# Kernel tuning notes

Hardware: AMD Instinct MI355X
Metric: run time of the kernel (lower is better)

Reference implementation:

```python
import jax, jax.numpy as jnp
import numpy as np

BS, S, N, C, H, CP, T, CT, NB = 1, 2, 2048, 128, 8, 16, 512, 384, 3
DH = C // H
INF = 1.0e8

def _ln(x, w, b, eps=1e-5):
    mu = jnp.mean(x, axis=-1, keepdims=True)
    var = jnp.var(x, axis=-1, keepdims=True)
    return (x - mu) * jax.lax.rsqrt(var + eps) * w + b

def _ln_na(x, eps=1e-5):
    mu = jnp.mean(x, axis=-1, keepdims=True)
    var = jnp.var(x, axis=-1, keepdims=True)
    return (x - mu) * jax.lax.rsqrt(var + eps)

def _betas(n):
    # query row l belongs to window centered at 32*(l//32)+16; keys within +/- n_keys//2=64
    l = jnp.arange(n)
    centers = (l // 32) * 32 + 16
    m = jnp.arange(n)
    ok = (m[None, :] >= (centers - 64)[:, None]) & (m[None, :] < (centers + 64)[:, None])
    return jnp.where(ok, 0.0, -INF).astype(jnp.float32)

def setup_inputs():
    key = jax.random.key(0)
    ks = iter(jax.random.split(key, 80))
    def W(*shape):
        return jax.random.normal(next(ks), shape, dtype=jnp.float32) * 0.05
    return {
        "atom_single": jax.random.normal(next(ks), (BS, S, N, C), dtype=jnp.float32),
        "atom_proj": jax.random.normal(next(ks), (BS, N, C), dtype=jnp.float32),
        "atom_pair": jax.random.normal(next(ks), (BS, N, N, CP), dtype=jnp.float32),
        "mask": jnp.ones((BS, N), jnp.float32),
        "tok_idx": jnp.sort(jax.random.randint(next(ks), (BS, N), 0, T), axis=-1),
        "aln_s_w": jnp.ones((NB, C), jnp.float32), "aln_s_b": jnp.zeros((NB, C), jnp.float32),
        "aln_gate_w": W(NB, C, C), "aln_gate_b": jnp.zeros((NB, C), jnp.float32),
        "aln_shift_w": W(NB, C, C),
        "q_w": W(NB, C, C), "q_b": jnp.zeros((NB, C), jnp.float32),
        "k_w": W(NB, C, C), "v_w": W(NB, C, C),
        "pair_ln_w": jnp.ones((NB, CP), jnp.float32), "pair_ln_b": jnp.zeros((NB, CP), jnp.float32),
        "pair_w": W(NB, CP, H),
        "gate_w": W(NB, C, C), "out_w": W(NB, C, C),
        "og_w": W(NB, C, C), "og_b": jnp.full((NB, C), -2.0, jnp.float32),
        "t_aln_s_w": jnp.ones((NB, C), jnp.float32), "t_aln_s_b": jnp.zeros((NB, C), jnp.float32),
        "t_aln_gate_w": W(NB, C, C), "t_aln_gate_b": jnp.zeros((NB, C), jnp.float32),
        "t_aln_shift_w": W(NB, C, C),
        "t_a_w": W(NB, C, 2 * C), "t_b_w": W(NB, C, 2 * C),
        "t_out_w": W(NB, 2 * C, C),
        "t_og_w": W(NB, C, C), "t_og_b": jnp.full((NB, C), -2.0, jnp.float32),
        "tok_w": W(C, CT),
    }

def _forward(atom_single, atom_proj, atom_pair, mask, tok_idx, aln_s_w, aln_s_b, aln_gate_w, aln_gate_b, aln_shift_w, q_w, q_b, k_w, v_w, pair_ln_w, pair_ln_b, pair_w, gate_w, out_w, og_w, og_b, t_aln_s_w, t_aln_s_b, t_aln_gate_w, t_aln_gate_b, t_aln_shift_w, t_a_w, t_b_w, t_out_w, t_og_w, t_og_b, tok_w):
    betas = _betas(N)[None, None, None]                        # [1,1,1,N,N]
    mask_bias = ((mask - 1.0) * INF)[:, None, None, None, :]   # [bs,1,1,1,N]
    s = atom_proj[:, None]                                     # [bs,1,N,C]
    a = atom_single                                            # [bs,S,N,C]
    for i in range(NB):
        # AttentionPairBias with AdaLN conditioning on s
        sn = _ln(s, aln_s_w[i], aln_s_b[i])
        a1 = jax.nn.sigmoid(sn @ aln_gate_w[i] + aln_gate_b[i]) * _ln_na(a) + sn @ aln_shift_w[i]
        q = (a1 @ q_w[i] + q_b[i]).reshape(BS, S, N, H, DH)
        k = (a1 @ k_w[i]).reshape(BS, S, N, H, DH)
        v = (a1 @ v_w[i]).reshape(BS, S, N, H, DH)
        zb = _ln(atom_pair, pair_ln_w[i], pair_ln_b[i]) @ pair_w[i]    # [bs,N,N,H]
        zb = jnp.transpose(zb, (0, 3, 1, 2))[:, None]                  # [bs,1,H,N,N]
        logits = jnp.einsum('bsqhd,bskhd->bshqk', q, k) / np.float32(np.sqrt(DH)) + zb + betas + mask_bias
        p = jax.nn.softmax(logits, axis=-1)
        o = jnp.einsum('bshqk,bskhd->bsqhd', p, v).reshape(BS, S, N, C)
        o = (jax.nn.sigmoid(a1 @ gate_w[i]) * o) @ out_w[i]
        a = a + jax.nn.sigmoid(sn @ og_w[i] + og_b[i]) * o
        # ConditionedTransitionBlock (SwiGLU with adaLN-Zero gating)
        sn2 = _ln(s, t_aln_s_w[i], t_aln_s_b[i])
        a2 = jax.nn.sigmoid(sn2 @ t_aln_gate_w[i] + t_aln_gate_b[i]) * _ln_na(a) + sn2 @ t_aln_shift_w[i]
        hidden = jax.nn.silu(a2 @ t_a_w[i]) * (a2 @ t_b_w[i])
        a = a + jax.nn.sigmoid(sn2 @ t_og_w[i] + t_og_b[i]) * (hidden @ t_out_w[i])
    # project to token dim, relu, scatter-mean atoms -> tokens
    q_tok = jax.nn.relu(a @ tok_w)                             # [bs,S,N,CT]
    oh = jax.nn.one_hot(tok_idx, T, dtype=q_tok.dtype)         # [bs,N,T]
    cnt = jnp.clip(jnp.sum(oh, axis=1), 1.0)                   # [bs,T]
    tok = jnp.einsum('bsnc,bnt->bstc', q_tok, oh) / cnt[:, None, :, None]
    return tok

def reference(atom_single, atom_proj, atom_pair, mask, tok_idx, aln_s_w, aln_s_b, aln_gate_w, aln_gate_b, aln_shift_w, q_w, q_b, k_w, v_w, pair_ln_w, pair_ln_b, pair_w, gate_w, out_w, og_w, og_b, t_aln_s_w, t_aln_s_b, t_aln_gate_w, t_aln_gate_b, t_aln_shift_w, t_a_w, t_b_w, t_out_w, t_og_w, t_og_b, tok_w):
    return _forward(atom_single, atom_proj, atom_pair, mask, tok_idx, aln_s_w, aln_s_b, aln_gate_w, aln_gate_b, aln_shift_w, q_w, q_b, k_w, v_w, pair_ln_w, pair_ln_b, pair_w, gate_w, out_w, og_w, og_b, t_aln_s_w, t_aln_s_b, t_aln_gate_w, t_aln_gate_b, t_aln_shift_w, t_a_w, t_b_w, t_out_w, t_og_w, t_og_b, tok_w)
```

## Files before the change

### kernel.cpp

```cpp
#include <hip/hip_runtime.h>
#include <math.h>

#define NATOM 2048
#define CD 128
#define SD 2
#define TT 512
#define CTD 384
#define NBI 3
#define MR 4096

typedef unsigned short ushortx;
typedef __attribute__((ext_vector_type(8))) short bf16x8;
typedef __attribute__((ext_vector_type(4))) float f32x4;
typedef __attribute__((ext_vector_type(4))) unsigned short us4;

__device__ __forceinline__ float sigm(float x){ return 1.0f/(1.0f+expf(-x)); }
__device__ __forceinline__ ushortx f2b(float f){
  union { float f; unsigned u; } v; v.f = f;
  unsigned r = v.u + 0x7fffu + ((v.u>>16)&1u);
  return (ushortx)(r>>16);
}
__device__ __forceinline__ float b2f(ushortx u){
  union { unsigned u; float f; } v; v.u = ((unsigned)u)<<16; return v.f;
}
union U8 { ushortx u[8]; float4 v; };

__device__ __forceinline__ void unpack8(float* dst, float4 v){
  U8 pk; pk.v = v;
  #pragma unroll
  for (int t=0;t<8;t++) dst[t] = b2f(pk.u[t]);
}

#define OFFB_W3T    0ll
#define OFFB_B3     589824ll
#define OFFB_WQKVGT 599040ll
#define OFFB_BQ     992256ll
#define OFFB_WOUTT  998400ll
#define OFFB_WABT   1096704ll
#define OFFB_WTOUTT 1489920ll
#define OFFB_WTOKT  1686528ll
#define OFFB_A1     1784832ll
#define OFFB_SNP    2833408ll
#define OFFB_A      12270592ll
#define OFFB_QKVG   14367744ll
#define OFFB_ZB     18562048ll
#define OFFB_QTOK   31144960ll

struct WPtrs {
  const float *aln_gate_w, *aln_gate_b, *aln_shift_w, *og_w, *og_b;
  const float *t_aln_gate_w, *t_aln_gate_b, *t_aln_shift_w, *t_og_w, *t_og_b;
  const float *q_w, *q_b, *k_w, *v_w, *gate_w, *out_w;
  const float *t_a_w, *t_b_w, *t_out_w, *tok_w;
};

__global__ __launch_bounds__(256) void prologue_kernel(WPtrs P, char* __restrict__ wsb,
  const float* __restrict__ atom_single, const float* __restrict__ atom_pair,
  const float* __restrict__ plw, const float* __restrict__ plb, const float* __restrict__ pw)
{
  int b = blockIdx.x;
  if (b < 3471){
    long long idx = (long long)b*256 + threadIdx.x;
    const long long s0=294912, s1=2304, s2=196608, s3=1536, s4=49152, s5=196608, s6=98304;
    if (idx < s0) {
      int which = (int)(idx/49152); int r = (int)(idx%49152); int n=r/128, k=r%128;
      int i = which>>1, t = which&1;
      const float* src;
      if (n<128)      src = (t?P.t_aln_gate_w :P.aln_gate_w ) + i*16384 + k*128 + n;
      else if (n<256) src = (t?P.t_aln_shift_w:P.aln_shift_w) + i*16384 + k*128 + (n-128);
      else            src = (t?P.t_og_w       :P.og_w       ) + i*16384 + k*128 + (n-256);
      ((ushortx*)(wsb+OFFB_W3T))[idx] = f2b(*src); return;
    }
    idx -= s0;
    if (idx < s1) {
      int which = (int)(idx/384); int col = (int)(idx%384); int i=which>>1, t=which&1;
      float v = 0.f;
      if (col<128)       v = (t?P.t_aln_gate_b:P.aln_gate_b)[i*128+col];
      else if (col>=256) v = (t?P.t_og_b      :P.og_b      )[i*128+col-256];
      ((float*)(wsb+OFFB_B3))[idx] = v; return;
    }
    idx -= s1;
    if (idx < s2) {
      int i = (int)(idx/65536); int r = (int)(idx%65536); int n=r/128, k=r%128;
      int seg = n>>7, c = n&127;
      const float* src = (seg==0?P.q_w: seg==1?P.k_w: seg==2?P.v_w: P.gate_w) + i*16384 + k*128 + c;
      ((ushortx*)(wsb+OFFB_WQKVGT))[idx] = f2b(*src); return;
    }
    idx -= s2;
    if (idx < s3) {
      int i = (int)(idx/512); int col = (int)(idx%512);
      ((float*)(wsb+OFFB_BQ))[idx] = (col<128) ? P.q_b[i*128+col] : 0.f; return;
    }
    idx -= s3;
    if (idx < s4) {
      int i = (int)(idx/16384); int r = (int)(idx%16384); int n=r/128, k=r%128;
      ((ushortx*)(wsb+OFFB_WOUTT))[idx] = f2b(P.out_w[i*16384 + k*128 + n]); return;
    }
    idx -= s4;
    if (idx < s5) {
      int i = (int)(idx/65536); int r = (int)(idx%65536); int n=r/128, k=r%128;
      const float* src = (n<256) ? P.t_a_w + i*32768 + k*256 + n
                                 : P.t_b_w + i*32768 + k*256 + (n-256);
      ((ushortx*)(wsb+OFFB_WABT))[idx] = f2b(*src); return;
    }
    idx -= s5;
    if (idx < s6) {
      int i = (int)(idx/32768); int r = (int)(idx%32768); int n=r/256, k=r%256;
      ((ushortx*)(wsb+OFFB_WTOUTT))[idx] = f2b(P.t_out_w[i*32768 + k*128 + n]); return;
    }
    idx -= s6;
    {
      int n = (int)(idx/128); int k = (int)(idx%128);
      ((ushortx*)(wsb+OFFB_WTOKT))[idx] = f2b(P.tok_w[k*384 + n]); return;
    }
  }
  if (b < 5519){
    int i = (b-3471)*256 + threadIdx.x;
    ((float*)(wsb+OFFB_A))[i] = atom_single[i];
    return;
  }
  {
    int idx = (b-5519)*256 + threadIdx.x;
    int q = idx>>7, j = idx&127;
    int m = (q & ~31) - 48 + j;
    bool ok = (m>=0 && m<NATOM);
    float x[16]; float mu=0.f, rs=0.f;
    if (ok){
      float s=0.f, sq=0.f;
      const float* p = atom_pair + ((long long)q*NATOM + m)*16;
      #pragma unroll
      for (int c=0;c<16;c++){ x[c]=p[c]; s+=x[c]; sq+=x[c]*x[c]; }
      mu = s*(1.f/16.f); float var = sq*(1.f/16.f)-mu*mu; rs = rsqrtf(var+1e-5f);
    }
    ushortx* zb = (ushortx*)(wsb+OFFB_ZB);
    #pragma unroll
    for (int it=0; it<NBI; it++){
      float out[8] = {0,0,0,0,0,0,0,0};
      if (ok){
        #pragma unroll
        for (int c=0;c<16;c++){
          float xn = (x[c]-mu)*rs*plw[it*16+c] + plb[it*16+c];
          #pragma unroll
          for (int h=0;h<8;h++) out[h] += xn * pw[it*128 + c*8 + h];
        }
      }
      #pragma unroll
      for (int h=0;h<8;h++)
        zb[(((long long)it*8+h)*NATOM + q)*128 + j] = f2b(out[h]);
    }
  }
}

__global__ __launch_bounds__(256) void attn_kernel(const ushortx* __restrict__ qkvg,
  const ushortx* __restrict__ zb, const float* __restrict__ mask, ushortx* __restrict__ og)
{
  int qb = blockIdx.x, h = blockIdx.y, s = blockIdx.z;
  int base = qb*32 - 48;
  __shared__ __align__(16) float Qs[32][20];
  __shared__ __align__(16) ushortx KsU[128][24];
  __shared__ __align__(16) ushortx VsU[128][24];
  __shared__ __align__(16) float Ls[32][132];
  __shared__ float maskb[128], redx[32][8], rowv[32];
  int tid = threadIdx.x;
  for (int idx=tid; idx<32*2; idx+=256){
    int r=idx>>1, d8=(idx&1)*8;
    float4 v = *(const float4*)&qkvg[((long long)(s*NATOM + qb*32 + r))*512 + h*16 + d8];
    unpack8(&Qs[r][d8], v);
  }
  for (int idx=tid; idx<512; idx+=256){
    int j = idx&127, d8 = ((idx>>7)&1)*8, kv = idx>>8;
    int m = base + j; int mc = m<0?0:(m>NATOM-1?NATOM-1:m);
    long long row = ((long long)(s*NATOM + mc))*512;
    float4 v = *(const float4*)&qkvg[row + (kv?256:128) + h*16 + d8];
    if (kv) *(float4*)&VsU[j][d8] = v; else *(float4*)&KsU[j][d8] = v;
  }
  if (tid < 128){
    int m = base + tid;
    maskb[tid] = (m>=0 && m<NATOM) ? (mask[m]-1.0f)*1e8f : -1e30f;
  }
  __syncthreads();
  int r = tid>>3, g = tid&7;
  {
    float4 q0=*(float4*)&Qs[r][0], q1=*(float4*)&Qs[r][4], q2=*(float4*)&Qs[r][8], q3=*(float4*)&Qs[r][12];
    const ushortx* zrow = zb + ((long long)h*NATOM + (qb*32+r))*128;
    #pragma unroll
    for (int j=g; j<128; j+=8){
      U8 ka, kb; ka.v = *(const float4*)&KsU[j][0]; kb.v = *(const float4*)&KsU[j][8];
      float dot = q0.x*b2f(ka.u[0]) + q0.y*b2f(ka.u[1]) + q0.z*b2f(ka.u[2]) + q0.w*b2f(ka.u[3])
                + q1.x*b2f(ka.u[4]) + q1.y*b2f(ka.u[5]) + q1.z*b2f(ka.u[6]) + q1.w*b2f(ka.u[7])
                + q2.x*b2f(kb.u[0]) + q2.y*b2f(kb.u[1]) + q2.z*b2f(kb.u[2]) + q2.w*b2f(kb.u[3])
                + q3.x*b2f(kb.u[4]) + q3.y*b2f(kb.u[5]) + q3.z*b2f(kb.u[6]) + q3.w*b2f(kb.u[7]);
      Ls[r][j] = dot*0.25f + b2f(zrow[j]) + maskb[j];
    }
  }
  __syncthreads();
  float pmax = -1e30f;
  for (int j=g*16; j<g*16+16; j++) pmax = fmaxf(pmax, Ls[r][j]);
  redx[r][g] = pmax; __syncthreads();
  if (g==0){ float mx=redx[r][0]; for(int u=1;u<8;u++) mx=fmaxf(mx,redx[r][u]); rowv[r]=mx; }
  __syncthreads();
  float mx = rowv[r];
  float psum = 0.f;
  for (int j=g*16; j<g*16+16; j++){ float e = expf(Ls[r][j]-mx); Ls[r][j]=e; psum += e; }
  redx[r][g] = psum; __syncthreads();
  if (g==0){ float sm=0.f; for(int u=0;u<8;u++) sm+=redx[r][u]; rowv[r]=sm; }
  __syncthreads();
  {
    int q2=tid>>3, dg=(tid>>1)&3, jh=tid&1;
    float4 acc = make_float4(0.f,0.f,0.f,0.f);
    for (int j=jh*64; j<jh*64+64; j++){
      float p = Ls[q2][j];
      us4 vv = *(const us4*)&VsU[j][dg*4];
      acc.x += p*b2f(vv[0]); acc.y += p*b2f(vv[1]);
      acc.z += p*b2f(vv[2]); acc.w += p*b2f(vv[3]);
    }
    acc.x += __shfl_xor(acc.x,1); acc.y += __shfl_xor(acc.y,1);
    acc.z += __shfl_xor(acc.z,1); acc.w += __shfl_xor(acc.w,1);
    if (jh==0){
      long long mrow = (long long)(s*NATOM + qb*32 + q2);
      float inv = 1.0f / rowv[q2];
      us4 gt = *(const us4*)&qkvg[mrow*512 + 384 + h*16 + dg*4];
      us4 st;
      st[0] = f2b(sigm(b2f(gt[0]))*acc.x*inv);
      st[1] = f2b(sigm(b2f(gt[1]))*acc.y*inv);
      st[2] = f2b(sigm(b2f(gt[2]))*acc.z*inv);
      st[3] = f2b(sigm(b2f(gt[3]))*acc.w*inv);
      *(us4*)(og + mrow*128 + h*16 + dg*4) = st;
    }
  }
}

template<int LAST>
__global__ __launch_bounds__(256) void postattn_kernel(
  float* __restrict__ Af, const ushortx* __restrict__ A1,
  const ushortx* __restrict__ Wout,
  const ushortx* __restrict__ Wab,
  const ushortx* __restrict__ Wtout,
  const ushortx* __restrict__ WN,
  const float*   __restrict__ biasN,
  const ushortx* __restrict__ snpA,
  const ushortx* __restrict__ snpT,
  const ushortx* __restrict__ snpN,
  ushortx* __restrict__ QKVG,
  float*   __restrict__ QTOK)
{
  __shared__ __align__(16) ushortx Bt[2][64][136];
  __shared__ __align__(16) float   Afr[16][132];
  __shared__ __align__(16) ushortx A2t[16][136];
  __shared__ __align__(16) ushortx Ht[16][264];
  __shared__ __align__(16) ushortx XX[16*264];
  ushortx (*A1t)[136] = (ushortx(*)[136])XX;
  ushortx (*Hs)[264]  = (ushortx(*)[264])XX;

  int tid=threadIdx.x, rowBase=blockIdx.x*16;
  int wave=tid>>6, lane=tid&63, lr=lane&15, lk=(lane>>4)*8;
  int wc = wave*16;
  int r=tid>>4, c8=(tid&15)*8;
  long long grow = rowBase + r;
  int sr=tid>>2, csB=(tid&3)*32;
  int crow = (lane>>4)*4;

  *(float4*)&A1t[r][c8] = *(const float4*)&A1[grow*128 + c8];
  { const float4* ap=(const float4*)&Af[grow*128+c8];
    *(float4*)&Afr[r][c8]=ap[0]; *(float4*)&Afr[r][c8+4]=ap[1]; }
  const int NP = LAST ? 20 : 22;
  {
    const float4* bg = (const float4*)(Wout + (long long)sr*128 + csB);
    #pragma unroll
    for (int u=0;u<4;u++) *(float4*)&Bt[0][sr][csB+u*8] = bg[u];
  }
  f32x4 acc = (f32x4){0.f,0.f,0.f,0.f};
  for (int p=0; p<NP; p++){
    __syncthreads();
    if (p+1 < NP){
      int pn = p+1;
      const ushortx* bsrc; long long bstride;
      if (pn<2)      { bsrc = Wout  + (long long)(pn*64)*128;                      bstride=128; }
      else if (pn<10){ bsrc = Wab   + (long long)((pn-2)*64)*128;                  bstride=128; }
      else if (pn<14){ int q=pn-10; bsrc = Wtout + (long long)((q>>1)*64)*256 + (q&1)*128; bstride=256; }
      else           { int q=pn-14; bsrc = WN    + (long long)(q*64)*128;          bstride=128; }
      const float4* bg=(const float4*)(bsrc + (long long)sr*bstride + csB);
      #pragma unroll
      for (int u=0;u<4;u++) *(float4*)&Bt[pn&1][sr][csB+u*8] = bg[u];
    }
    if (p==2){
      float x[8], s=0.f, sq=0.f;
      #pragma unroll
      for (int u=0;u<8;u++){ x[u]=Afr[r][c8+u]; s+=x[u]; sq+=x[u]*x[u]; }
      #pragma unroll
      for (int off=1; off<16; off<<=1){ s+=__shfl_xor(s,off); sq+=__shfl_xor(sq,off); }
      float mu=s*(1.f/128.f), rs=rsqrtf(sq*(1.f/128.f)-mu*mu+1e-5f);
      const ushortx* sp = snpT + (long long)(grow&2047)*384;
      U8 ga,ha,pk; ga.v=*(const float4*)&sp[c8]; ha.v=*(const float4*)&sp[128+c8];
      #pragma unroll
      for (int t=0;t<8;t++) pk.u[t]=f2b(sigm(b2f(ga.u[t]))*((x[t]-mu)*rs)+b2f(ha.u[t]));
      *(float4*)&A2t[r][c8]=pk.v;
      __syncthreads();
    }
    if (p==14){
      float x[8], s=0.f, sq=0.f;
      #pragma unroll
      for (int u=0;u<8;u++){ x[u]=Afr[r][c8+u]; s+=x[u]; sq+=x[u]*x[u]; }
      { float4* ap=(float4*)&Af[grow*128+c8];
        ap[0]=*(float4*)&Afr[r][c8]; ap[1]=*(float4*)&Afr[r][c8+4]; }
      if (LAST){
        U8 pk;
        #pragma unroll
        for (int t=0;t<8;t++) pk.u[t]=f2b(x[t]);
        *(float4*)&A2t[r][c8]=pk.v;
      } else {
        #pragma unroll
        for (int off=1; off<16; off<<=1){ s+=__shfl_xor(s,off); sq+=__shfl_xor(sq,off); }
        float mu=s*(1.f/128.f), rs=rsqrtf(sq*(1.f/128.f)-mu*mu+1e-5f);
        const ushortx* sp = snpN + (long long)(grow&2047)*384;
        U8 ga,ha,pk; ga.v=*(const float4*)&sp[c8]; ha.v=*(const float4*)&sp[128+c8];
        #pragma unroll
        for (int t=0;t<8;t++) pk.u[t]=f2b(sigm(b2f(ga.u[t]))*((x[t]-mu)*rs)+b2f(ha.u[t]));
        *(float4*)&A2t[r][c8]=pk.v;
      }
      __syncthreads();
    }
    if (p!=11 && p!=13) acc=(f32x4){0.f,0.f,0.f,0.f};
    #pragma unroll
    for (int ks=0; ks<4; ks++){
      bf16x8 a;
      if (p<2)       a = *(const bf16x8*)&A1t[lr][ks*32+lk];
      else if (p<10) a = *(const bf16x8*)&A2t[lr][ks*32+lk];
      else if (p<14){ int kc=(p-10)&1; a = *(const bf16x8*)&Hs[lr][kc*128+ks*32+lk]; }
      else           a = *(const bf16x8*)&A2t[lr][ks*32+lk];
      bf16x8 b = *(const bf16x8*)&Bt[p&1][wc+lr][ks*32+lk];
      acc = __builtin_amdgcn_mfma_f32_16x16x32_bf16(a,b,acc,0,0,0);
    }
    if (p<2){
      int ccol = p*64 + wc + lr;
      #pragma unroll
      for (int rr=0;rr<4;rr++){
        int rrow=crow+rr;
        float g=b2f(snpA[(long long)((rowBase+rrow)&2047)*384 + 256 + ccol]);
        Afr[rrow][ccol]+=sigm(g)*acc[rr];
      }
    } else if (p<10){
      int cp=p-2; int ccol=cp*64+wc+lr;
      if (cp<4){
        #pragma unroll
        for (int rr=0;rr<4;rr++) Ht[crow+rr][ccol]=f2b(acc[rr]);
      } else {
        int hc=ccol-256;
        #pragma unroll
        for (int rr=0;rr<4;rr++){
          float ha=b2f(Ht[crow+rr][hc]);
          Hs[crow+rr][hc]=f2b(ha*sigm(ha)*acc[rr]);
        }
      }
    } else if (p==11 || p==13){
      int cp=(p-10)>>1; int ccol=cp*64+wc+lr;
      #pragma unroll
      for (int rr=0;rr<4;rr++){
        int rrow=crow+rr;
        float g=b2f(snpT[(long long)((rowBase+rrow)&2047)*384 + 256 + ccol]);
        Afr[rrow][ccol]+=sigm(g)*acc[rr];
      }
    } else if (p>=14){
      int q=p-14; int ccol=q*64+wc+lr;
      if (LAST){
        #pragma unroll
        for (int rr=0;rr<4;rr++)
          QTOK[(long long)(rowBase+crow+rr)*384 + ccol]=fmaxf(acc[rr],0.f);
      } else {
        float bv=biasN[ccol];
        #pragma unroll
        for (int rr=0;rr<4;rr++)
          QKVG[(long long)(rowBase+crow+rr)*512 + ccol]=f2b(acc[rr]+bv);
      }
    }
  }
}

template<int AM, int BM>
__global__ __launch_bounds__(256) void gemm_f(
    const void* __restrict__ Asrc, long long strideA,
    const ushortx* __restrict__ B, long long strideB,
    const float* __restrict__ bias, long long strideBias,
    void* Cv, long long strideC,
    int M, int N, int K, int mode,
    const ushortx* __restrict__ gate, int gate_ld, int gate_coloff,
    const void* __restrict__ p1, const void* __restrict__ p2,
    const void* __restrict__ p3, const void* __restrict__ p4)
{
  constexpr int CG  = 256/BM;
  constexpr int XC  = 128/CG;
  constexpr int F4  = XC/8;
  constexpr int ACI = BM/32;
  int z = blockIdx.z;
  B += z*strideB;
  if (bias) bias += z*strideBias;
  float* C = (float*)Cv + z*strideC;
  ushortx* Cu = (ushortx*)Cv + z*strideC;
  __shared__ __align__(16) ushortx At[BM][136];
  __shared__ __align__(16) ushortx Bt[64][136];
  int tid = threadIdx.x;
  int rowBase = blockIdx.y*BM, colBase = blockIdx.x*64;
  int wave = tid>>6, lane = tid&63;
  int wr = (wave>>1)*(BM/2), wc = (wave&1)*32;
  int lr = lane&15, lk = (lane>>4)*8;
  f32x4 acc[ACI][2];
  #pragma unroll
  for (int i=0;i<ACI;i++)
    #pragma unroll
    for (int j=0;j<2;j++) acc[i][j] = (f32x4){0.f,0.f,0.f,0.f};

  int sr = tid/CG, q = tid%CG, cs = q*XC;
  int row = rowBase + sr;
  int bsr = tid>>2, bq = tid&3, bcs = bq*32;

  for (int kc=0; kc<K; kc+=128){
    if (kc) __syncthreads();
    if (AM==0){
      const ushortx* Ab = (const ushortx*)Asrc + z*strideA;
      const float4* ag = (const float4*)(Ab + (long long)row*K + kc + cs);
      #pragma unroll
      for (int u=0;u<F4;u++) *(float4*)&At[sr][cs+u*8] = ag[u];
    } else if (AM==3){
      const float* Af_ = (const float*)Asrc;
      const float4* ar = (const float4*)(Af_ + (long long)row*128 + cs);
      #pragma unroll
      for (int u=0;u<F4;u++){
        float4 a = ar[2*u], b = ar[2*u+1];
        U8 pk;
        pk.u[0]=f2b(a.x); pk.u[1]=f2b(a.y); pk.u[2]=f2b(a.z); pk.u[3]=f2b(a.w);
        pk.u[4]=f2b(b.x); pk.u[5]=f2b(b.y); pk.u[6]=f2b(b.z); pk.u[7]=f2b(b.w);
        *(float4*)&At[sr][cs+u*8] = pk.v;
      }
    } else {
      const float* arow = (const float*)Asrc + (long long)row*128;
      float x[XC]; float s=0.f, sq=0.f;
      const float4* ar = (const float4*)(arow + cs);
      #pragma unroll
      for (int u=0;u<XC/4;u++){
        float4 t = ar[u];
        x[4*u]=t.x; x[4*u+1]=t.y; x[4*u+2]=t.z; x[4*u+3]=t.w;
        s += t.x+t.y+t.z+t.w;
        sq += t.x*t.x+t.y*t.y+t.z*t.z+t.w*t.w;
      }
      #pragma unroll
      for (int off=1; off<CG; off<<=1){ s += __shfl_xor(s,off); sq += __shfl_xor(sq,off); }
      float mu = s*(1.f/128.f), var = sq*(1.f/128.f)-mu*mu;
      float rs = rsqrtf(var + 1e-5f);
      if (AM==1){
        const ushortx* sp = (const ushortx*)p1 + (long long)(row & (NATOM-1))*384;
        const float4* gr = (const float4*)(sp + cs);
        const float4* hr = (const float4*)(sp + 128 + cs);
        #pragma unroll
        for (int u=0;u<F4;u++){
          U8 ga, ha, pk;
          ga.v = gr[u]; ha.v = hr[u];
          #pragma unroll
          for (int t=0;t<8;t++)
            pk.u[t] = f2b(sigm(b2f(ga.u[t]))*((x[8*u+t]-mu)*rs) + b2f(ha.u[t]));
          *(float4*)&At[sr][cs+u*8] = pk.v;
        }
      } else {
        int iw = z>>1, tw = z&1;
        const float* w = (const float*)(tw?p3:p1) + iw*128;
        const float* b = (const float*)(tw?p4:p2) + iw*128;
        const float4* wrp = (const float4*)(w + cs);
        const float4* brp = (const float4*)(b + cs);
        #pragma unroll
        for (int u=0;u<F4;u++){
          float4 wa = wrp[2*u], wb = wrp[2*u+1];
          float4 ba = brp[2*u], bb = brp[2*u+1];
          U8 pk;
          pk.u[0]=f2b((x[8*u  ]-mu)*rs*wa.x+ba.x);
          pk.u[1]=f2b((x[8*u+1]-mu)*rs*wa.y+ba.y);
          pk.u[2]=f2b((x[8*u+2]-mu)*rs*wa.z+ba.z);
          pk.u[3]=f2b((x[8*u+3]-mu)*rs*wa.w+ba.w);
          pk.u[4]=f2b((x[8*u+4]-mu)*rs*wb.x+bb.x);
          pk.u[5]=f2b((x[8*u+5]-mu)*rs*wb.y+bb.y);
          pk.u[6]=f2b((x[8*u+6]-mu)*rs*wb.z+bb.z);
          pk.u[7]=f2b((x[8*u+7]-mu)*rs*wb.w+bb.w);
          *(float4*)&At[sr][cs+u*8] = pk.v;
        }
      }
    }
    {
      const float4* bg = (const float4*)(B + (long long)(colBase+bsr)*K + kc + bcs);
      #pragma unroll
      for (int u=0;u<4;u++) *(float4*)&Bt[bsr][bcs+u*8] = bg[u];
    }
    __syncthreads();
    #pragma unroll
    for (int ks=0; ks<4; ks++){
      bf16x8 b0 = *(const bf16x8*)&Bt[wc+lr][ks*32+lk];
      bf16x8 b1 = *(const bf16x8*)&Bt[wc+16+lr][ks*32+lk];
      #pragma unroll
      for (int i=0;i<ACI;i++){
        bf16x8 a = *(const bf16x8*)&At[wr+i*16+lr][ks*32+lk];
        acc[i][0] = __builtin_amdgcn_mfma_f32_16x16x32_bf16(a,b0,acc[i][0],0,0,0);
        acc[i][1] = __builtin_amdgcn_mfma_f32_16x16x32_bf16(a,b1,acc[i][1],0,0,0);
      }
    }
  }
  int crow0 = rowBase + wr + (lane>>4)*4;
  int ccol0 = colBase + wc + lr;
  #pragma unroll
  for (int i=0;i<ACI;i++){
    #pragma unroll
    for (int j=0;j<2;j++){
      int col = ccol0 + j*16;
      float bv = bias ? bias[col] : 0.f;
      #pragma unroll
      for (int rr=0; rr<4; rr++){
        int rrow = crow0 + i*16 + rr;
        float v = acc[i][j][rr] + bv;
        long long ci = (long long)rrow*N + col;
        if (mode==1) C[ci] = fmaxf(v, 0.f);
        else if (mode==2){
          int n = rrow & (NATOM-1);
          C[ci] += sigm(b2f(gate[(long long)n*gate_ld + gate_coloff + col])) * v;
        } else if (mode==3) Cu[ci] = f2b(v);
        else if (mode==4) Cu[ci] = f2b(fmaxf(v, 0.f));
        else C[ci] = v;
      }
    }
  }
}

__global__ __launch_bounds__(128) void tokagg_kernel(const int* __restrict__ tok_idx,
    const float* __restrict__ qtok, float* __restrict__ out)
{
  int t = blockIdx.x;
  int lo=0, hi=NATOM;
  while (lo<hi){ int mid=(lo+hi)>>1; if (tok_idx[mid] < t) lo=mid+1; else hi=mid; }
  int start = lo;
  lo = start; hi = NATOM;
  while (lo<hi){ int mid=(lo+hi)>>1; if (tok_idx[mid] <= t) lo=mid+1; else hi=mid; }
  int end = lo;
  int cnt = end - start;
  float inv = 1.0f / (float)(cnt>0 ? cnt : 1);
  for (int s=0; s<SD; s++)
    for (int c=threadIdx.x; c<CTD; c+=128){
      float acc = 0.f;
      for (int n=start; n<end; n++) acc += qtok[((long long)(s*NATOM+n))*CTD + c];
      out[(long long)(s*TT + t)*CTD + c] = acc*inv;
    }
}

extern "C" void kernel_launch(void* const* d_in, const int* in_sizes, int n_in,
                              void* d_out, int out_size, void* d_ws, size_t ws_size,
                              hipStream_t stream)
{
  const float* atom_single = (const float*)d_in[0];
  const float* atom_proj   = (const float*)d_in[1];
  const float* atom_pair   = (const float*)d_in[2];
  const float* mask        = (const float*)d_in[3];
  const int*   tok_idx     = (const int*)  d_in[4];
  const float* aln_s_w     = (const float*)d_in[5];
  const float* aln_s_b     = (const float*)d_in[6];
  const float* pair_ln_w   = (const float*)d_in[14];
  const float* pair_ln_b   = (const float*)d_in[15];
  const float* pair_w      = (const float*)d_in[16];
  const float* t_aln_s_w   = (const float*)d_in[21];
  const float* t_aln_s_b   = (const float*)d_in[22];

  char* wsb = (char*)d_ws;
  ushortx* W3T    = (ushortx*)(wsb+OFFB_W3T);
  float*   B3     = (float*)  (wsb+OFFB_B3);
  ushortx* WQKVGT = (ushortx*)(wsb+OFFB_WQKVGT);
  float*   BQ     = (float*)  (wsb+OFFB_BQ);
  ushortx* WOUTT  = (ushortx*)(wsb+OFFB_WOUTT);
  ushortx* WABT   = (ushortx*)(wsb+OFFB_WABT);
  ushortx* WTOUTT = (ushortx*)(wsb+OFFB_WTOUTT);
  ushortx* WTOKT  = (ushortx*)(wsb+OFFB_WTOKT);
  ushortx* A1     = (ushortx*)(wsb+OFFB_A1);
  ushortx* SNP    = (ushortx*)(wsb+OFFB_SNP);
  float*   Af     = (float*)  (wsb+OFFB_A);
  ushortx* QKVG   = (ushortx*)(wsb+OFFB_QKVG);
  ushortx* ZB     = (ushortx*)(wsb+OFFB_ZB);
  float*   QTOK   = (float*)  (wsb+OFFB_QTOK);

  WPtrs P;
  P.aln_gate_w=(const float*)d_in[7];  P.aln_gate_b=(const float*)d_in[8];  P.aln_shift_w=(const float*)d_in[9];
  P.og_w=(const float*)d_in[19]; P.og_b=(const float*)d_in[20];
  P.t_aln_gate_w=(const float*)d_in[23]; P.t_aln_gate_b=(const float*)d_in[24]; P.t_aln_shift_w=(const float*)d_in[25];
  P.t_og_w=(const float*)d_in[29]; P.t_og_b=(const float*)d_in[30];
  P.q_w=(const float*)d_in[10]; P.q_b=(const float*)d_in[11]; P.k_w=(const float*)d_in[12];
  P.v_w=(const float*)d_in[13]; P.gate_w=(const float*)d_in[17]; P.out_w=(const float*)d_in[18];
  P.t_a_w=(const float*)d_in[26]; P.t_b_w=(const float*)d_in[27]; P.t_out_w=(const float*)d_in[28];
  P.tok_w=(const float*)d_in[31];

  prologue_kernel<<<6543,256,0,stream>>>(P, wsb, atom_single, atom_pair,
      pair_ln_w, pair_ln_b, pair_w);
  gemm_f<4,64><<<dim3(6,32,6),256,0,stream>>>(atom_proj, 0, W3T, 49152ll,
      B3, 384ll, SNP, 786432ll, NATOM, 384, 128, 3, nullptr, 0, 0,
      aln_s_w, aln_s_b, t_aln_s_w, t_aln_s_b);
  gemm_f<1,64><<<dim3(8,64,1),256,0,stream>>>(Af, 0, WQKVGT, 0,
      BQ, 0, QKVG, 0, MR, 512, 128, 3, nullptr, 0, 0,
      SNP, nullptr, nullptr, nullptr);

  for (int i=0;i<NBI;i++){
    const ushortx* snpA = SNP + (long long)(2*i)*786432;
    const ushortx* snpT = SNP + (long long)(2*i+1)*786432;
    attn_kernel<<<dim3(64,8,2),256,0,stream>>>(QKVG, ZB + (long long)i*2097152, mask, A1);
    if (i < NBI-1){
      postattn_kernel<0><<<256,256,0,stream>>>(Af, A1,
          WOUTT + (long long)i*16384, WABT + (long long)i*65536, WTOUTT + (long long)i*32768,
          WQKVGT + (long long)(i+1)*65536, BQ + (long long)(i+1)*512,
          snpA, snpT, SNP + (long long)(2*(i+1))*786432, QKVG, nullptr);
    } else {
      postattn_kernel<1><<<256,256,0,stream>>>(Af, A1,
          WOUTT + (long long)i*16384, WABT + (long long)i*65536, WTOUTT + (long long)i*32768,
          WTOKT, nullptr, snpA, snpT, nullptr, nullptr, QTOK);
    }
  }
  tokagg_kernel<<<TT,128,0,stream>>>(tok_idx, QTOK, (float*)d_out);
}
```

Before: 533.8 us.

## Fuse local attention into post-attention kernel with double-buffered QKVG

Drops the separate attention kernel and computes the windowed attention for each 16-row block inside the post-attention kernel. Per-head K/V/Z/Q/G tiles are prefetched into double-buffered shared memory while the previous head is computed, and the gated output stays in shared memory instead of going through a global A1 buffer. QKVG is ping-ponged between two buffers, because other blocks still read the current iteration's K/V while new values are being written. The atom_single copy in the prologue is removed by reading the input directly, and SNP rows are staged once into shared memory. Only 256 blocks now do the attention work, down from 1024, and the larger shared-memory footprint may lower occupancy.

```diff
diff --git a/kernel.cpp b/kernel.cpp
--- a/kernel.cpp
+++ b/kernel.cpp
@@ -25,12 +25,6 @@
 }
 union U8 { ushortx u[8]; float4 v; };
 
-__device__ __forceinline__ void unpack8(float* dst, float4 v){
-  U8 pk; pk.v = v;
-  #pragma unroll
-  for (int t=0;t<8;t++) dst[t] = b2f(pk.u[t]);
-}
-
 #define OFFB_W3T    0ll
 #define OFFB_B3     589824ll
 #define OFFB_WQKVGT 599040ll
@@ -39,12 +33,12 @@
 #define OFFB_WABT   1096704ll
 #define OFFB_WTOUTT 1489920ll
 #define OFFB_WTOKT  1686528ll
-#define OFFB_A1     1784832ll
 #define OFFB_SNP    2833408ll
 #define OFFB_A      12270592ll
 #define OFFB_QKVG   14367744ll
 #define OFFB_ZB     18562048ll
 #define OFFB_QTOK   31144960ll
+#define OFFB_QKVG2  37436416ll
 
 struct WPtrs {
   const float *aln_gate_w, *aln_gate_b, *aln_shift_w, *og_w, *og_b;
@@ -54,7 +48,7 @@
 };
 
 __global__ __launch_bounds__(256) void prologue_kernel(WPtrs P, char* __restrict__ wsb,
-  const float* __restrict__ atom_single, const float* __restrict__ atom_pair,
+  const float* __restrict__ atom_pair,
   const float* __restrict__ plw, const float* __restrict__ plb, const float* __restrict__ pw)
 {
   int b = blockIdx.x;
@@ -113,13 +107,8 @@
       ((ushortx*)(wsb+OFFB_WTOKT))[idx] = f2b(P.tok_w[k*384 + n]); return;
     }
   }
-  if (b < 5519){
-    int i = (b-3471)*256 + threadIdx.x;
-    ((float*)(wsb+OFFB_A))[i] = atom_single[i];
-    return;
-  }
   {
-    int idx = (b-5519)*256 + threadIdx.x;
+    int idx = (b-3471)*256 + threadIdx.x;
     int q = idx>>7, j = idx&127;
     int m = (q & ~31) - 48 + j;
     bool ok = (m>=0 && m<NATOM);
@@ -150,88 +139,13 @@
   }
 }
 
-__global__ __launch_bounds__(256) void attn_kernel(const ushortx* __restrict__ qkvg,
-  const ushortx* __restrict__ zb, const float* __restrict__ mask, ushortx* __restrict__ og)
-{
-  int qb = blockIdx.x, h = blockIdx.y, s = blockIdx.z;
-  int base = qb*32 - 48;
-  __shared__ __align__(16) float Qs[32][20];
-  __shared__ __align__(16) ushortx KsU[128][24];
-  __shared__ __align__(16) ushortx VsU[128][24];
-  __shared__ __align__(16) float Ls[32][132];
-  __shared__ float maskb[128], redx[32][8], rowv[32];
-  int tid = threadIdx.x;
-  for (int idx=tid; idx<32*2; idx+=256){
-    int r=idx>>1, d8=(idx&1)*8;
-    float4 v = *(const float4*)&qkvg[((long long)(s*NATOM + qb*32 + r))*512 + h*16 + d8];
-    unpack8(&Qs[r][d8], v);
-  }
-  for (int idx=tid; idx<512; idx+=256){
-    int j = idx&127, d8 = ((idx>>7)&1)*8, kv = idx>>8;
-    int m = base + j; int mc = m<0?0:(m>NATOM-1?NATOM-1:m);
-    long long row = ((long long)(s*NATOM + mc))*512;
-    float4 v = *(const float4*)&qkvg[row + (kv?256:128) + h*16 + d8];
-    if (kv) *(float4*)&VsU[j][d8] = v; else *(float4*)&KsU[j][d8] = v;
-  }
-  if (tid < 128){
-    int m = base + tid;
-    maskb[tid] = (m>=0 && m<NATOM) ? (mask[m]-1.0f)*1e8f : -1e30f;
-  }
-  __syncthreads();
-  int r = tid>>3, g = tid&7;
-  {
-    float4 q0=*(float4*)&Qs[r][0], q1=*(float4*)&Qs[r][4], q2=*(float4*)&Qs[r][8], q3=*(float4*)&Qs[r][12];
-    const ushortx* zrow = zb + ((long long)h*NATOM + (qb*32+r))*128;
-    #pragma unroll
-    for (int j=g; j<128; j+=8){
-      U8 ka, kb; ka.v = *(const float4*)&KsU[j][0]; kb.v = *(const float4*)&KsU[j][8];
-      float dot = q0.x*b2f(ka.u[0]) + q0.y*b2f(ka.u[1]) + q0.z*b2f(ka.u[2]) + q0.w*b2f(ka.u[3])
-                + q1.x*b2f(ka.u[4]) + q1.y*b2f(ka.u[5]) + q1.z*b2f(ka.u[6]) + q1.w*b2f(ka.u[7])
-                + q2.x*b2f(kb.u[0]) + q2.y*b2f(kb.u[1]) + q2.z*b2f(kb.u[2]) + q2.w*b2f(kb.u[3])
-                + q3.x*b2f(kb.u[4]) + q3.y*b2f(kb.u[5]) + q3.z*b2f(kb.u[6]) + q3.w*b2f(kb.u[7]);
-      Ls[r][j] = dot*0.25f + b2f(zrow[j]) + maskb[j];
-    }
-  }
-  __syncthreads();
-  float pmax = -1e30f;
-  for (int j=g*16; j<g*16+16; j++) pmax = fmaxf(pmax, Ls[r][j]);
-  redx[r][g] = pmax; __syncthreads();
-  if (g==0){ float mx=redx[r][0]; for(int u=1;u<8;u++) mx=fmaxf(mx,redx[r][u]); rowv[r]=mx; }
-  __syncthreads();
-  float mx = rowv[r];
-  float psum = 0.f;
-  for (int j=g*16; j<g*16+16; j++){ float e = expf(Ls[r][j]-mx); Ls[r][j]=e; psum += e; }
-  redx[r][g] = psum; __syncthreads();
-  if (g==0){ float sm=0.f; for(int u=0;u<8;u++) sm+=redx[r][u]; rowv[r]=sm; }
-  __syncthreads();
-  {
-    int q2=tid>>3, dg=(tid>>1)&3, jh=tid&1;
-    float4 acc = make_float4(0.f,0.f,0.f,0.f);
-    for (int j=jh*64; j<jh*64+64; j++){
-      float p = Ls[q2][j];
-      us4 vv = *(const us4*)&VsU[j][dg*4];
-      acc.x += p*b2f(vv[0]); acc.y += p*b2f(vv[1]);
-      acc.z += p*b2f(vv[2]); acc.w += p*b2f(vv[3]);
-    }
-    acc.x += __shfl_xor(acc.x,1); acc.y += __shfl_xor(acc.y,1);
-    acc.z += __shfl_xor(acc.z,1); acc.w += __shfl_xor(acc.w,1);
-    if (jh==0){
-      long long mrow = (long long)(s*NATOM + qb*32 + q2);
-      float inv = 1.0f / rowv[q2];
-      us4 gt = *(const us4*)&qkvg[mrow*512 + 384 + h*16 + dg*4];
-      us4 st;
-      st[0] = f2b(sigm(b2f(gt[0]))*acc.x*inv);
-      st[1] = f2b(sigm(b2f(gt[1]))*acc.y*inv);
-      st[2] = f2b(sigm(b2f(gt[2]))*acc.z*inv);
-      st[3] = f2b(sigm(b2f(gt[3]))*acc.w*inv);
-      *(us4*)(og + mrow*128 + h*16 + dg*4) = st;
-    }
-  }
-}
-
 template<int LAST>
-__global__ __launch_bounds__(256) void postattn_kernel(
-  float* __restrict__ Af, const ushortx* __restrict__ A1,
+__global__ __launch_bounds__(256) void fused_iter(
+  const float* __restrict__ Afsrc,
+  float* __restrict__ Af,
+  const ushortx* __restrict__ QKVGin,
+  const ushortx* __restrict__ zb,
+  const float* __restrict__ mask,
   const ushortx* __restrict__ Wout,
   const ushortx* __restrict__ Wab,
   const ushortx* __restrict__ Wtout,
@@ -240,7 +154,7 @@
   const ushortx* __restrict__ snpA,
   const ushortx* __restrict__ snpT,
   const ushortx* __restrict__ snpN,
-  ushortx* __restrict__ QKVG,
+  ushortx* __restrict__ QKVGout,
   float*   __restrict__ QTOK)
 {
   __shared__ __align__(16) ushortx Bt[2][64][136];
@@ -248,26 +162,117 @@
   __shared__ __align__(16) ushortx A2t[16][136];
   __shared__ __align__(16) ushortx Ht[16][264];
   __shared__ __align__(16) ushortx XX[16*264];
+  __shared__ __align__(16) ushortx Kh[2][128][24];
+  __shared__ __align__(16) ushortx Vh[2][128][24];
+  __shared__ __align__(16) ushortx Zh[2][16][136];
+  __shared__ __align__(16) ushortx Qh[2][16][16];
+  __shared__ __align__(16) ushortx Gh[2][16][16];
+  __shared__ __align__(16) float   Ls[16][132];
+  __shared__ __align__(16) ushortx SnpT[16][392];
+  __shared__ __align__(16) ushortx SnpN[16][392];
+  __shared__ __align__(16) ushortx SnpAog[16][136];
+  __shared__ float maskb[128];
   ushortx (*A1t)[136] = (ushortx(*)[136])XX;
   ushortx (*Hs)[264]  = (ushortx(*)[264])XX;
 
-  int tid=threadIdx.x, rowBase=blockIdx.x*16;
+  int tid = threadIdx.x, rowBase = blockIdx.x*16;
+  int sIdx = rowBase >> 11;
+  int n0 = rowBase & 2047;
+  int wbase = (n0 & ~31) - 48;
   int wave=tid>>6, lane=tid&63, lr=lane&15, lk=(lane>>4)*8;
   int wc = wave*16;
-  int r=tid>>4, c8=(tid&15)*8;
+  int r = tid>>4, tcol = tid&15, c8 = tcol*8;
   long long grow = rowBase + r;
   int sr=tid>>2, csB=(tid&3)*32;
   int crow = (lane>>4)*4;
 
-  *(float4*)&A1t[r][c8] = *(const float4*)&A1[grow*128 + c8];
-  { const float4* ap=(const float4*)&Af[grow*128+c8];
+  { const float4* ap=(const float4*)&Afsrc[grow*128+c8];
     *(float4*)&Afr[r][c8]=ap[0]; *(float4*)&Afr[r][c8+4]=ap[1]; }
-  const int NP = LAST ? 20 : 22;
+  if (tid < 128){
+    int m = wbase + tid;
+    maskb[tid] = (m>=0 && m<NATOM) ? (mask[m]-1.0f)*1e8f : -1e30f;
+  }
+  #pragma unroll
+  for (int k=0;k<3;k++){ int idx=tid+k*256; int rr=idx/48, cc=(idx%48)*8;
+    *(float4*)&SnpT[rr][cc] = *(const float4*)&snpT[(long long)((rowBase+rr)&2047)*384 + cc]; }
+  if (!LAST){
+    #pragma unroll
+    for (int k=0;k<3;k++){ int idx=tid+k*256; int rr=idx/48, cc=(idx%48)*8;
+      *(float4*)&SnpN[rr][cc] = *(const float4*)&snpN[(long long)((rowBase+rr)&2047)*384 + cc]; }
+  }
+  *(float4*)&SnpAog[r][c8] = *(const float4*)&snpA[(long long)((rowBase+r)&2047)*384 + 256 + c8];
   {
     const float4* bg = (const float4*)(Wout + (long long)sr*128 + csB);
     #pragma unroll
     for (int u=0;u<4;u++) *(float4*)&Bt[0][sr][csB+u*8] = bg[u];
   }
+
+  int jr=tid>>1, hf=tid&1;
+  int mm=wbase+jr; int mc = mm<0?0:(mm>NATOM-1?NATOM-1:mm);
+  long long krow = ((long long)(sIdx*NATOM+mc))*512;
+  auto issue = [&](int h, float4&kreg, float4&vreg, float4&zreg, float4&qg){
+    kreg = *(const float4*)&QKVGin[krow + 128 + h*16 + hf*8];
+    vreg = *(const float4*)&QKVGin[krow + 256 + h*16 + hf*8];
+    zreg = *(const float4*)&zb[((long long)h*NATOM + n0 + r)*128 + c8];
+    if (tid < 32)
+      qg = *(const float4*)&QKVGin[((long long)(rowBase+(tid>>1)))*512 + h*16 + (tid&1)*8];
+    else if (tid < 64){
+      int tt=tid-32;
+      qg = *(const float4*)&QKVGin[((long long)(rowBase+(tt>>1)))*512 + 384 + h*16 + (tt&1)*8];
+    }
+  };
+  auto commit = [&](int bb, float4 kreg, float4 vreg, float4 zreg, float4 qg){
+    *(float4*)&Kh[bb][jr][hf*8] = kreg;
+    *(float4*)&Vh[bb][jr][hf*8] = vreg;
+    *(float4*)&Zh[bb][r][c8] = zreg;
+    if (tid < 32) *(float4*)&Qh[bb][tid>>1][(tid&1)*8] = qg;
+    else if (tid < 64){ int tt=tid-32; *(float4*)&Gh[bb][tt>>1][(tt&1)*8] = qg; }
+  };
+  { float4 k0,v0,z0,q0 = make_float4(0,0,0,0);
+    issue(0,k0,v0,z0,q0); commit(0,k0,v0,z0,q0); }
+  __syncthreads();
+  for (int h=0; h<8; ++h){
+    int bb=h&1;
+    float4 kn,vn,zn,qn = make_float4(0,0,0,0);
+    if (h<7) issue(h+1,kn,vn,zn,qn);
+    float qv[16];
+    { U8 qa,qb_;
+      qa.v=*(const float4*)&Qh[bb][r][0]; qb_.v=*(const float4*)&Qh[bb][r][8];
+      #pragma unroll
+      for (int t=0;t<8;t++){ qv[t]=b2f(qa.u[t]); qv[8+t]=b2f(qb_.u[t]); } }
+    float lv[8], pmax=-1e30f;
+    #pragma unroll
+    for (int u=0;u<8;u++){
+      int j=tcol+u*16;
+      U8 ka,kb_;
+      ka.v=*(const float4*)&Kh[bb][j][0]; kb_.v=*(const float4*)&Kh[bb][j][8];
+      float dot=0.f;
+      #pragma unroll
+      for (int t=0;t<8;t++) dot += qv[t]*b2f(ka.u[t]);
+      #pragma unroll
+      for (int t=0;t<8;t++) dot += qv[8+t]*b2f(kb_.u[t]);
+      float L = dot*0.25f + b2f(Zh[bb][r][j]) + maskb[j];
+      lv[u]=L; pmax=fmaxf(pmax,L);
+    }
+    #pragma unroll
+    for (int off=1; off<16; off<<=1) pmax = fmaxf(pmax, __shfl_xor(pmax,off));
+    float ps=0.f;
+    #pragma unroll
+    for (int u=0;u<8;u++){ float e=expf(lv[u]-pmax); Ls[r][tcol+u*16]=e; ps+=e; }
+    #pragma unroll
+    for (int off=1; off<16; off<<=1) ps += __shfl_xor(ps,off);
+    float inv = 1.0f/ps;
+    __syncthreads();
+    float a0=0.f;
+    #pragma unroll 4
+    for (int j=0;j<128;j++) a0 += Ls[r][j]*b2f(Vh[bb][j][tcol]);
+    float gt = b2f(Gh[bb][r][tcol]);
+    A1t[r][h*16+tcol] = f2b(sigm(gt)*a0*inv);
+    if (h<7) commit((h+1)&1,kn,vn,zn,qn);
+    __syncthreads();
+  }
+
+  const int NP = LAST ? 20 : 22;
   f32x4 acc = (f32x4){0.f,0.f,0.f,0.f};
   for (int p=0; p<NP; p++){
     __syncthreads();
@@ -289,8 +294,8 @@
       #pragma unroll
       for (int off=1; off<16; off<<=1){ s+=__shfl_xor(s,off); sq+=__shfl_xor(sq,off); }
       float mu=s*(1.f/128.f), rs=rsqrtf(sq*(1.f/128.f)-mu*mu+1e-5f);
-      const ushortx* sp = snpT + (long long)(grow&2047)*384;
-      U8 ga,ha,pk; ga.v=*(const float4*)&sp[c8]; ha.v=*(const float4*)&sp[128+c8];
+      U8 ga,ha,pk;
+      ga.v=*(const float4*)&SnpT[r][c8]; ha.v=*(const float4*)&SnpT[r][128+c8];
       #pragma unroll
       for (int t=0;t<8;t++) pk.u[t]=f2b(sigm(b2f(ga.u[t]))*((x[t]-mu)*rs)+b2f(ha.u[t]));
       *(float4*)&A2t[r][c8]=pk.v;
@@ -311,8 +316,8 @@
         #pragma unroll
         for (int off=1; off<16; off<<=1){ s+=__shfl_xor(s,off); sq+=__shfl_xor(sq,off); }
         float mu=s*(1.f/128.f), rs=rsqrtf(sq*(1.f/128.f)-mu*mu+1e-5f);
-        const ushortx* sp = snpN + (long long)(grow&2047)*384;
-        U8 ga,ha,pk; ga.v=*(const float4*)&sp[c8]; ha.v=*(const float4*)&sp[128+c8];
+        U8 ga,ha,pk;
+        ga.v=*(const float4*)&SnpN[r][c8]; ha.v=*(const float4*)&SnpN[r][128+c8];
         #pragma unroll
         for (int t=0;t<8;t++) pk.u[t]=f2b(sigm(b2f(ga.u[t]))*((x[t]-mu)*rs)+b2f(ha.u[t]));
         *(float4*)&A2t[r][c8]=pk.v;
@@ -335,7 +340,7 @@
       #pragma unroll
       for (int rr=0;rr<4;rr++){
         int rrow=crow+rr;
-        float g=b2f(snpA[(long long)((rowBase+rrow)&2047)*384 + 256 + ccol]);
+        float g=b2f(SnpAog[rrow][ccol]);
         Afr[rrow][ccol]+=sigm(g)*acc[rr];
       }
     } else if (p<10){
@@ -356,7 +361,7 @@
       #pragma unroll
       for (int rr=0;rr<4;rr++){
         int rrow=crow+rr;
-        float g=b2f(snpT[(long long)((rowBase+rrow)&2047)*384 + 256 + ccol]);
+        float g=b2f(SnpT[rrow][256+ccol]);
         Afr[rrow][ccol]+=sigm(g)*acc[rr];
       }
     } else if (p>=14){
@@ -369,7 +374,7 @@
         float bv=biasN[ccol];
         #pragma unroll
         for (int rr=0;rr<4;rr++)
-          QKVG[(long long)(rowBase+crow+rr)*512 + ccol]=f2b(acc[rr]+bv);
+          QKVGout[(long long)(rowBase+crow+rr)*512 + ccol]=f2b(acc[rr]+bv);
       }
     }
   }
@@ -382,7 +387,6 @@
     const float* __restrict__ bias, long long strideBias,
     void* Cv, long long strideC,
     int M, int N, int K, int mode,
-    const ushortx* __restrict__ gate, int gate_ld, int gate_coloff,
     const void* __restrict__ p1, const void* __restrict__ p2,
     const void* __restrict__ p3, const void* __restrict__ p4)
 {
@@ -414,23 +418,7 @@
 
   for (int kc=0; kc<K; kc+=128){
     if (kc) __syncthreads();
-    if (AM==0){
-      const ushortx* Ab = (const ushortx*)Asrc + z*strideA;
-      const float4* ag = (const float4*)(Ab + (long long)row*K + kc + cs);
-      #pragma unroll
-      for (int u=0;u<F4;u++) *(float4*)&At[sr][cs+u*8] = ag[u];
-    } else if (AM==3){
-      const float* Af_ = (const float*)Asrc;
-      const float4* ar = (const float4*)(Af_ + (long long)row*128 + cs);
-      #pragma unroll
-      for (int u=0;u<F4;u++){
-        float4 a = ar[2*u], b = ar[2*u+1];
-        U8 pk;
-        pk.u[0]=f2b(a.x); pk.u[1]=f2b(a.y); pk.u[2]=f2b(a.z); pk.u[3]=f2b(a.w);
-        pk.u[4]=f2b(b.x); pk.u[5]=f2b(b.y); pk.u[6]=f2b(b.z); pk.u[7]=f2b(b.w);
-        *(float4*)&At[sr][cs+u*8] = pk.v;
-      }
-    } else {
+    {
       const float* arow = (const float*)Asrc + (long long)row*128;
       float x[XC]; float s=0.f, sq=0.f;
       const float4* ar = (const float4*)(arow + cs);
@@ -512,13 +500,8 @@
         int rrow = crow0 + i*16 + rr;
         float v = acc[i][j][rr] + bv;
         long long ci = (long long)rrow*N + col;
-        if (mode==1) C[ci] = fmaxf(v, 0.f);
-        else if (mode==2){
-          int n = rrow & (NATOM-1);
-          C[ci] += sigm(b2f(gate[(long long)n*gate_ld + gate_coloff + col])) * v;
-        } else if (mode==3) Cu[ci] = f2b(v);
-        else if (mode==4) Cu[ci] = f2b(fmaxf(v, 0.f));
-        else C[ci] = v;
+        Cu[ci] = f2b(v);
+        (void)C; (void)mode;
       }
     }
   }
@@ -570,10 +553,10 @@
   ushortx* WABT   = (ushortx*)(wsb+OFFB_WABT);
   ushortx* WTOUTT = (ushortx*)(wsb+OFFB_WTOUTT);
   ushortx* WTOKT  = (ushortx*)(wsb+OFFB_WTOKT);
-  ushortx* A1     = (ushortx*)(wsb+OFFB_A1);
   ushortx* SNP    = (ushortx*)(wsb+OFFB_SNP);
   float*   Af     = (float*)  (wsb+OFFB_A);
   ushortx* QKVG   = (ushortx*)(wsb+OFFB_QKVG);
+  ushortx* QKVG2  = (ushortx*)(wsb+OFFB_QKVG2);
   ushortx* ZB     = (ushortx*)(wsb+OFFB_ZB);
   float*   QTOK   = (float*)  (wsb+OFFB_QTOK);
 
@@ -587,28 +570,35 @@
   P.t_a_w=(const float*)d_in[26]; P.t_b_w=(const float*)d_in[27]; P.t_out_w=(const float*)d_in[28];
   P.tok_w=(const float*)d_in[31];
 
-  prologue_kernel<<<6543,256,0,stream>>>(P, wsb, atom_single, atom_pair,
+  prologue_kernel<<<4495,256,0,stream>>>(P, wsb, atom_pair,
       pair_ln_w, pair_ln_b, pair_w);
   gemm_f<4,64><<<dim3(6,32,6),256,0,stream>>>(atom_proj, 0, W3T, 49152ll,
-      B3, 384ll, SNP, 786432ll, NATOM, 384, 128, 3, nullptr, 0, 0,
+      B3, 384ll, SNP, 786432ll, NATOM, 384, 128, 3,
       aln_s_w, aln_s_b, t_aln_s_w, t_aln_s_b);
-  gemm_f<1,64><<<dim3(8,64,1),256,0,stream>>>(Af, 0, WQKVGT, 0,
-      BQ, 0, QKVG, 0, MR, 512, 128, 3, nullptr, 0, 0,
+  gemm_f<1,64><<<dim3(8,64,1),256,0,stream>>>(atom_single, 0, WQKVGT, 0,
+      BQ, 0, QKVG, 0, MR, 512, 128, 3,
       SNP, nullptr, nullptr, nullptr);
 
   for (int i=0;i<NBI;i++){
     const ushortx* snpA = SNP + (long long)(2*i)*786432;
     const ushortx* snpT = SNP + (long long)(2*i+1)*786432;
-    attn_kernel<<<dim3(64,8,2),256,0,stream>>>(QKVG, ZB + (long long)i*2097152, mask, A1);
+    ushortx* qin  = (i&1) ? QKVG2 : QKVG;
+    ushortx* qout = (i&1) ? QKVG  : QKVG2;
+    const float* afsrc = (i==0) ? atom_single : Af;
     if (i < NBI-1){
-      postattn_kernel<0><<<256,256,0,stream>>>(Af, A1,
+      fused_iter<0><<<256,256,0,stream>>>(afsrc, Af, qin,
+          ZB + (long long)i*2097152, mask,
           WOUTT + (long long)i*16384, WABT + (long long)i*65536, WTOUTT + (long long)i*32768,
           WQKVGT + (long long)(i+1)*65536, BQ + (long long)(i+1)*512,
-          snpA, snpT, SNP + (long long)(2*(i+1))*786432, QKVG, nullptr);
+          snpA, snpT, SNP + (long long)(2*(i+1))*786432,
+          qout, nullptr);
     } else {
-      postattn_kernel<1><<<256,256,0,stream>>>(Af, A1,
+      fused_iter<1><<<256,256,0,stream>>>(afsrc, Af, qin,
+          ZB + (long long)i*2097152, mask,
           WOUTT + (long long)i*16384, WABT + (long long)i*65536, WTOUTT + (long long)i*32768,
-          WTOKT, nullptr, snpA, snpT, nullptr, nullptr, QTOK);
+          WTOKT, nullptr,
+          snpA, snpT, nullptr,
+          qout, QTOK);
     }
   }
   tokagg_kernel<<<TT,128,0,stream>>>(tok_idx, QTOK, (float*)d_out);
```

Measured after the change: 579.6 us. +8.6%, slower.
